# Kernel tuning notes

Measured on AMD Instinct MI355X. Metric: run time of the kernel, lower is better.

## Reference

```python
import jax, jax.numpy as jnp
import numpy as np

N = 50000
IN_CHNL = 128
OUT_CHNL = 64
HEADS = 2
NEG_SLOPE = 0.2  # PyG GATConv default leaky_relu slope


def gat_conv(x, W, a_src, a_dst, bias, edge_index):
    """PyG-style GATConv (concat=True, add_self_loops=True, eval mode).
    x: [N, F_in], W: [F_in, H*C], a_src/a_dst: [H, C], bias: [H*C],
    edge_index: [2, E] (row 0 = src, row 1 = dst)."""
    n = x.shape[0]
    loops = jnp.arange(n, dtype=edge_index.dtype)
    src = jnp.concatenate([edge_index[0], loops])
    dst = jnp.concatenate([edge_index[1], loops])

    h = (x @ W).reshape(n, HEADS, OUT_CHNL)          # [N, H, C]
    s_src = jnp.einsum('nhc,hc->nh', h, a_src)       # [N, H]
    s_dst = jnp.einsum('nhc,hc->nh', h, a_dst)       # [N, H]

    e = s_src[src] + s_dst[dst]                      # [E', H]
    e = jax.nn.leaky_relu(e, NEG_SLOPE)
    # segment softmax over destination neighborhoods
    e_max = jax.ops.segment_max(e, dst, num_segments=n)
    e_max = jnp.where(jnp.isfinite(e_max), e_max, 0.0)
    e_exp = jnp.exp(e - e_max[dst])
    denom = jax.ops.segment_sum(e_exp, dst, num_segments=n)
    alpha = e_exp / denom[dst]                       # [E', H]

    msg = h[src] * alpha[:, :, None]                 # [E', H, C]
    out = jax.ops.segment_sum(msg, dst, num_segments=n)  # [N, H, C]
    return out.reshape(n, HEADS * OUT_CHNL) + bias


def setup_inputs() -> dict:
    key = jax.random.key(0)
    ks = jax.random.split(key, 12)
    node_h = jax.random.normal(ks[0], (N, IN_CHNL), dtype=jnp.float32)
    edge_index_pc = jax.random.randint(ks[1], (2, 600000), 0, N, dtype=jnp.int64 if jax.config.jax_enable_x64 else jnp.int32)
    edge_index_mc = jax.random.randint(ks[2], (2, 600000), 0, N, dtype=jnp.int64 if jax.config.jax_enable_x64 else jnp.int32)
    sc = 1.0 / np.sqrt(IN_CHNL)
    W_pc = jax.random.normal(ks[3], (IN_CHNL, HEADS * OUT_CHNL), dtype=jnp.float32) * sc
    a_src_pc = jax.random.normal(ks[4], (HEADS, OUT_CHNL), dtype=jnp.float32) * sc
    a_dst_pc = jax.random.normal(ks[5], (HEADS, OUT_CHNL), dtype=jnp.float32) * sc
    b_pc = jnp.zeros((HEADS * OUT_CHNL,), dtype=jnp.float32)
    W_mc = jax.random.normal(ks[6], (IN_CHNL, HEADS * OUT_CHNL), dtype=jnp.float32) * sc
    a_src_mc = jax.random.normal(ks[7], (HEADS, OUT_CHNL), dtype=jnp.float32) * sc
    a_dst_mc = jax.random.normal(ks[8], (HEADS, OUT_CHNL), dtype=jnp.float32) * sc
    b_mc = jnp.zeros((HEADS * OUT_CHNL,), dtype=jnp.float32)
    return {
        'node_h': node_h,
        'W_pc': W_pc, 'a_src_pc': a_src_pc, 'a_dst_pc': a_dst_pc, 'b_pc': b_pc,
        'W_mc': W_mc, 'a_src_mc': a_src_mc, 'a_dst_mc': a_dst_mc, 'b_mc': b_mc,
        'edge_index_pc': edge_index_pc, 'edge_index_mc': edge_index_mc,
    }


def reference(node_h, W_pc, a_src_pc, a_dst_pc, b_pc,
              W_mc, a_src_mc, a_dst_mc, b_mc,
              edge_index_pc, edge_index_mc):
    # eval mode: F.dropout is identity
    h_pc = jax.nn.elu(gat_conv(node_h, W_pc, a_src_pc, a_dst_pc, b_pc, edge_index_pc))
    h_mc = jax.nn.elu(gat_conv(node_h, W_mc, a_src_mc, a_dst_mc, b_mc, edge_index_mc))
    return 0.5 * (h_pc + h_mc)
```

## Files before the change

kernel.cpp:

```cpp
#include <hip/hip_runtime.h>
#include <hip/hip_bf16.h>

typedef unsigned int u32;
typedef unsigned short u16;
typedef long long i64;
typedef __bf16 bf16x8 __attribute__((ext_vector_type(8)));
typedef float f32x4 __attribute__((ext_vector_type(4)));

static constexpr int NN = 50000;
static constexpr int FI = 128;
static constexpr int FO = 128;
static constexpr int ER = 600000;
static constexpr int GLAB = 6272;
static constexpr int PROWS = 12544;
static constexpr int DSTRIDE = 38;
static constexpr int NQA = 1280;
static constexpr int ACS = (2 * ER + NQA - 1) / NQA;
static constexpr int NBIN = 128;
static constexpr int RBLK = 784;
static constexpr int LCAP = 24;
static constexpr int QCAPB = 10240;
static constexpr int GEMM_BLK = (NN + 63) / 64;
static constexpr float SLOPE = 0.2f;

__device__ __forceinline__ float bf2f(u16 u) {
  u32 x = ((u32)u) << 16;
  return __builtin_bit_cast(float, x);
}
__device__ __forceinline__ u16 f2bf(float f) {
  u32 u = __builtin_bit_cast(u32, f);
  u32 r = (u + 0x7fffu + ((u >> 16) & 1u)) >> 16;
  return (u16)r;
}
__device__ __forceinline__ float ldf(const void* p, size_t i, int isf32) {
  return isf32 ? ((const float*)p)[i] : bf2f(((const u16*)p)[i]);
}
__device__ __forceinline__ int lde(const void* p, size_t i, int is64) {
  return is64 ? (int)((const i64*)p)[i] : ((const int*)p)[i];
}

__device__ __forceinline__ void passA_body(const void* __restrict__ ei0,
                                           const void* __restrict__ ei1,
                                           int* __restrict__ qcurp,
                                           u32* __restrict__ qbuf, int bid) {
  __shared__ u32 lq[NBIN][LCAP];
  __shared__ int lcnt[NBIN];
  __shared__ int gbase[NBIN];
  __shared__ int s_i64;
  int tid = threadIdx.x;
  if (tid < NBIN) lcnt[tid] = 0;
  if (tid < 64) {
    u32 hi = (tid < 32) ? ((const u32*)ei0)[2 * tid + 1] : 1u;
    unsigned long long b2 = __ballot(hi == 0u);
    if (tid == 0) s_i64 = (__popcll(b2) >= 30) ? 1 : 0;
  }
  __syncthreads();
  int i64f = s_i64;
  int beg = bid * ACS;
  int end = min(beg + ACS, 2 * ER);
  for (int e = beg + tid; e < end; e += 256) {
    int g = e >= ER;
    int ee = e - g * ER;
    const void* ei = g ? ei1 : ei0;
    int d = lde(ei, (size_t)ER + ee, i64f);
    int s = lde(ei, (size_t)ee, i64f);
    s = min(max(s, 0), NN - 1);
    d = min(max(d, 0), NN - 1);
    int p = d & 7;
    int label = (d >> 3) + g * GLAB;
    int r = label / RBLK;
    int bin = p * 16 + r;
    int ll = label - r * RBLK;
    u32 entry = ((u32)s << 16) | (u32)ll;
    int pos = atomicAdd(&lcnt[bin], 1);
    if (pos < LCAP) {
      lq[bin][pos] = entry;
    } else {
      int idx = atomicAdd(&qcurp[bin * 16], 1);
      if (idx < QCAPB) qbuf[(size_t)bin * QCAPB + idx] = entry;
    }
  }
  __syncthreads();
  if (tid < NBIN) {
    int n = min(lcnt[tid], LCAP);
    lcnt[tid] = n;
    gbase[tid] = atomicAdd(&qcurp[tid * 16], n);
  }
  __syncthreads();
  int wv = tid >> 6, lane = tid & 63;
  for (int b = wv; b < NBIN; b += 4) {
    int n = lcnt[b];
    int gb = gbase[b];
    for (int i = lane; i < n; i += 64) {
      int idx = gb + i;
      if (idx < QCAPB) qbuf[(size_t)b * QCAPB + idx] = lq[b][i];
    }
  }
}

__global__ __launch_bounds__(256) void k1(
    const void* __restrict__ W0, const void* __restrict__ W1,
    const u32* __restrict__ x32, const void* __restrict__ ei0,
    const void* __restrict__ ei1, u16* __restrict__ wf,
    int* __restrict__ flags, int* __restrict__ qcurp, u32* __restrict__ qbuf) {
  int bid = blockIdx.x;
  int tid = threadIdx.x;
  if (bid < 16) {
    int lane = tid & 63;
    int chunk = bid * 4 + (tid >> 6);
    u32 e = (x32[lane] >> 23) & 0xffu;
    unsigned long long b1 = __ballot(e >= 118u && e <= 137u);
    int f32i = (__popcll(b1) >= 48) ? 1 : 0;
    int g = chunk >> 5, idx = chunk & 31;
    const void* W = g ? W1 : W0;
    int ks = idx >> 3, cg = idx & 7;
    int k0 = ks * 32 + (lane >> 4) * 8;
    int col = cg * 16 + (lane & 15);
    u16 v[8];
#pragma unroll
    for (int j = 0; j < 8; j++)
      v[j] = f2bf(ldf(W, (size_t)(k0 + j) * FO + col, f32i));
    u32 p0 = (u32)v[0] | ((u32)v[1] << 16);
    u32 p1 = (u32)v[2] | ((u32)v[3] << 16);
    u32 p2 = (u32)v[4] | ((u32)v[5] << 16);
    u32 p3 = (u32)v[6] | ((u32)v[7] << 16);
    *reinterpret_cast<uint4*>(wf + (size_t)(chunk * 64 + lane) * 8) =
        make_uint4(p0, p1, p2, p3);
    if (bid == 0 && tid < 64) {
      u32 hi = (tid < 32) ? ((const u32*)ei0)[2 * tid + 1] : 1u;
      unsigned long long b2 = __ballot(hi == 0u);
      if (tid == 0) {
        flags[0] = f32i;
        flags[1] = (__popcll(b2) >= 30) ? 1 : 0;
      }
    }
    return;
  }
  passA_body(ei0, ei1, qcurp, qbuf, bid - 16);
}

__global__ __launch_bounds__(256) void gemm2(
    const void* __restrict__ x, const u16* __restrict__ wf,
    u16* __restrict__ h0, u16* __restrict__ h1, const void* __restrict__ as0,
    const void* __restrict__ ad0, const void* __restrict__ as1,
    const void* __restrict__ ad1, float* __restrict__ ss,
    float* __restrict__ sd, const int* __restrict__ flags) {
  int f32i = flags[0];
  int g = blockIdx.x >= GEMM_BLK;
  int bid = blockIdx.x - g * GEMM_BLK;
  u16* h = g ? h1 : h0;
  const void* as = g ? as1 : as0;
  const void* ad = g ? ad1 : ad0;
  int tid = threadIdx.x;
  int lane = tid & 63, wv = tid >> 6;
  int rowbase = bid * 64 + wv * 16;
  int arow = rowbase + (lane & 15);
  if (arow >= NN) arow = NN - 1;
  int kg = lane >> 4;

  f32x4 acc[8];
#pragma unroll
  for (int i = 0; i < 8; i++) acc[i] = (f32x4){0.f, 0.f, 0.f, 0.f};

#pragma unroll
  for (int ks = 0; ks < 4; ks++) {
    uint4 q;
    if (f32i) {
      const float* xp = (const float*)x + (size_t)arow * FI + ks * 32 + kg * 8;
      float4 v0 = *reinterpret_cast<const float4*>(xp);
      float4 v1 = *reinterpret_cast<const float4*>(xp + 4);
      q.x = (u32)f2bf(v0.x) | ((u32)f2bf(v0.y) << 16);
      q.y = (u32)f2bf(v0.z) | ((u32)f2bf(v0.w) << 16);
      q.z = (u32)f2bf(v1.x) | ((u32)f2bf(v1.y) << 16);
      q.w = (u32)f2bf(v1.z) | ((u32)f2bf(v1.w) << 16);
    } else {
      q = *reinterpret_cast<const uint4*>((const u16*)x + (size_t)arow * FI +
                                          ks * 32 + kg * 8);
    }
    bf16x8 a = __builtin_bit_cast(bf16x8, q);
#pragma unroll
    for (int cg = 0; cg < 8; cg++) {
      bf16x8 b = __builtin_bit_cast(
          bf16x8, *reinterpret_cast<const uint4*>(
                      wf + (size_t)((g * 32 + ks * 8 + cg) * 64 + lane) * 8));
      acc[cg] = __builtin_amdgcn_mfma_f32_16x16x32_bf16(a, b, acc[cg], 0, 0, 0);
    }
  }
#pragma unroll
  for (int cg = 0; cg < 8; cg++) {
#pragma unroll
    for (int r = 0; r < 4; r++) {
      int orow = rowbase + kg * 4 + r;
      if (orow < NN)
        h[(size_t)orow * FO + cg * 16 + (lane & 15)] = f2bf(acc[cg][r]);
    }
  }
  float sa[2][4], sb[2][4];
#pragma unroll
  for (int i = 0; i < 2; i++)
#pragma unroll
    for (int r = 0; r < 4; r++) {
      sa[i][r] = 0.f;
      sb[i][r] = 0.f;
    }
#pragma unroll
  for (int cg = 0; cg < 8; cg++) {
    int c = cg * 16 + (lane & 15);
    float av = ldf(as, c, f32i);
    float dv = ldf(ad, c, f32i);
    int ih = cg >> 2;
#pragma unroll
    for (int r = 0; r < 4; r++) {
      sa[ih][r] += acc[cg][r] * av;
      sb[ih][r] += acc[cg][r] * dv;
    }
  }
#pragma unroll
  for (int i = 0; i < 2; i++)
#pragma unroll
    for (int r = 0; r < 4; r++)
#pragma unroll
      for (int off = 1; off <= 8; off <<= 1) {
        sa[i][r] += __shfl_xor(sa[i][r], off, 64);
        sb[i][r] += __shfl_xor(sb[i][r], off, 64);
      }
  if ((lane & 15) < 4) {
    int r = lane & 3;
    int row = rowbase + kg * 4 + r;
    if (row < NN) {
      reinterpret_cast<float2*>(ss)[(size_t)g * NN + row] =
          make_float2(sa[0][r], sa[1][r]);
      reinterpret_cast<float2*>(sd)[(size_t)g * NN + row] =
          make_float2(sb[0][r], sb[1][r]);
    }
  }
}

__global__ __launch_bounds__(256) void passB(const int* __restrict__ qcurp,
                                             const u32* __restrict__ qbuf,
                                             int* __restrict__ deg,
                                             u16* __restrict__ slots) {
  __shared__ int ldeg[RBLK];
  __shared__ u16 lslots[RBLK * DSTRIDE];
  int tid = threadIdx.x;
  int bin = blockIdx.x;
  int p = bin >> 4, r = bin & 15;
  for (int i = tid; i < RBLK; i += 256) {
    int lgl = r * RBLK + i;
    int g = lgl >= GLAB;
    int lg = lgl - g * GLAB;
    int dst = (lg << 3) | p;
    if (dst < NN) {
      ldeg[i] = 1;
      lslots[i * DSTRIDE] = (u16)dst;
    } else {
      ldeg[i] = 0;
    }
  }
  __syncthreads();
  int qn = min(qcurp[bin * 16], QCAPB);
  const u32* q = qbuf + (size_t)bin * QCAPB;
  for (int i = tid; i < qn; i += 256) {
    u32 pr = q[i];
    int ll = (int)(pr & 0xffffu);
    int old = atomicAdd(&ldeg[ll], 1);
    if (old < DSTRIDE) lslots[ll * DSTRIDE + old] = (u16)(pr >> 16);
  }
  __syncthreads();
  int rowbase = p * PROWS + r * RBLK;
  for (int i = tid; i < RBLK; i += 256) deg[rowbase + i] = min(ldeg[i], DSTRIDE);
  const u32* ls32 = reinterpret_cast<const u32*>(lslots);
  u32* gs32 = reinterpret_cast<u32*>(slots + (size_t)rowbase * DSTRIDE);
  for (int i = tid; i < RBLK * DSTRIDE / 2; i += 256) gs32[i] = ls32[i];
}

__global__ __launch_bounds__(256) void agg2(
    const u16* __restrict__ h0, const u16* __restrict__ h1,
    const float* __restrict__ ss, const float* __restrict__ sd,
    const int* __restrict__ deg, const u16* __restrict__ slots,
    const void* __restrict__ b0p, const void* __restrict__ b1p,
    void* __restrict__ outp, const int* __restrict__ flags) {
  int f32i = flags[0];
  int tid = threadIdx.x;
  int lane = tid & 63, wv = tid >> 6;
  int half = lane >> 5;
  int c = lane & 31;
  int dst = blockIdx.x * 8 + wv * 2 + half;
  int head = c >> 4;
  int hsh = head << 4;
  int hbase = half << 5;
  float res[2][4];
#pragma unroll
  for (int g = 0; g < 2; g++) {
    const uint2* hw = reinterpret_cast<const uint2*>(g ? h1 : h0);
    const float2* ss2 = reinterpret_cast<const float2*>(ss) + (size_t)g * NN;
    float2 sdv = reinterpret_cast<const float2*>(sd)[(size_t)g * NN + dst];
    int row = (dst & 7) * PROWS + g * GLAB + (dst >> 3);
    int n = min(deg[row], DSTRIDE);
    const u16* srow = slots + (size_t)row * DSTRIDE;
    int n1 = min(n, 32);
    int s1 = 0, s2 = 0;
    u32 pp1 = 0, pp2 = 0;
    float dp0 = 0.f, dp1 = 0.f;
    if (c < n1) {
      s1 = srow[c];
      float2 sv = ss2[s1];
      float e0 = sv.x + sdv.x, e1 = sv.y + sdv.y;
      e0 = (e0 > 0.f) ? e0 : SLOPE * e0;
      e1 = (e1 > 0.f) ? e1 : SLOPE * e1;
      float q0 = __expf(e0), q1 = __expf(e1);
      pp1 = (u32)f2bf(q0) | ((u32)f2bf(q1) << 16);
      dp0 += q0;
      dp1 += q1;
    }
    if (c + 32 < n) {
      s2 = srow[c + 32];
      float2 sv = ss2[s2];
      float e0 = sv.x + sdv.x, e1 = sv.y + sdv.y;
      e0 = (e0 > 0.f) ? e0 : SLOPE * e0;
      e1 = (e1 > 0.f) ? e1 : SLOPE * e1;
      float q0 = __expf(e0), q1 = __expf(e1);
      pp2 = (u32)f2bf(q0) | ((u32)f2bf(q1) << 16);
      dp0 += q0;
      dp1 += q1;
    }
#pragma unroll
    for (int off = 16; off >= 1; off >>= 1) {
      dp0 += __shfl_xor(dp0, off, 32);
      dp1 += __shfl_xor(dp1, off, 32);
    }
    float den = head ? dp1 : dp0;
    float a0 = 0.f, a1 = 0.f, a2 = 0.f, a3 = 0.f;
    int n1full = n1 & ~7;
    for (int b = 0; b < n1full; b += 8) {
      uint2 hv[8];
      float pv[8];
#pragma unroll
      for (int t = 0; t < 8; t++) {
        int sj = __shfl(s1, hbase + b + t, 64);
        u32 pp = __shfl(pp1, hbase + b + t, 64);
        pv[t] = bf2f((u16)(pp >> hsh));
        hv[t] = hw[(size_t)sj * 32 + c];
      }
#pragma unroll
      for (int t = 0; t < 8; t++) {
        a0 += pv[t] * bf2f((u16)hv[t].x);
        a1 += pv[t] * bf2f((u16)(hv[t].x >> 16));
        a2 += pv[t] * bf2f((u16)hv[t].y);
        a3 += pv[t] * bf2f((u16)(hv[t].y >> 16));
      }
    }
    if (n1full < n1) {
      uint2 hv[8];
      float pv[8];
#pragma unroll
      for (int t = 0; t < 8; t++) {
        int jj = (n1full + t < n1) ? (n1full + t) : n1full;
        int sj = __shfl(s1, hbase + jj, 64);
        u32 pp = __shfl(pp1, hbase + jj, 64);
        pv[t] = (n1full + t < n1) ? bf2f((u16)(pp >> hsh)) : 0.f;
        hv[t] = hw[(size_t)sj * 32 + c];
      }
#pragma unroll
      for (int t = 0; t < 8; t++) {
        a0 += pv[t] * bf2f((u16)hv[t].x);
        a1 += pv[t] * bf2f((u16)(hv[t].x >> 16));
        a2 += pv[t] * bf2f((u16)hv[t].y);
        a3 += pv[t] * bf2f((u16)(hv[t].y >> 16));
      }
    }
    if (n > 32) {
      int n2 = n - 32;
      for (int b = 0; b < n2; b += 8) {
        uint2 hv[8];
        float pv[8];
#pragma unroll
        for (int t = 0; t < 8; t++) {
          int jj = (b + t < n2) ? (b + t) : b;
          int sj = __shfl(s2, hbase + jj, 64);
          u32 pp = __shfl(pp2, hbase + jj, 64);
          pv[t] = (b + t < n2) ? bf2f((u16)(pp >> hsh)) : 0.f;
          hv[t] = hw[(size_t)sj * 32 + c];
        }
#pragma unroll
        for (int t = 0; t < 8; t++) {
          a0 += pv[t] * bf2f((u16)hv[t].x);
          a1 += pv[t] * bf2f((u16)(hv[t].x >> 16));
          a2 += pv[t] * bf2f((u16)hv[t].y);
          a3 += pv[t] * bf2f((u16)(hv[t].y >> 16));
        }
      }
    }
    float inv = (den > 0.f) ? 1.0f / den : 0.f;
    const void* bias = g ? b1p : b0p;
    float r0 = a0 * inv + ldf(bias, 4 * c + 0, f32i);
    float r1 = a1 * inv + ldf(bias, 4 * c + 1, f32i);
    float r2 = a2 * inv + ldf(bias, 4 * c + 2, f32i);
    float r3 = a3 * inv + ldf(bias, 4 * c + 3, f32i);
    res[g][0] = (r0 > 0.f) ? r0 : (__expf(r0) - 1.0f);
    res[g][1] = (r1 > 0.f) ? r1 : (__expf(r1) - 1.0f);
    res[g][2] = (r2 > 0.f) ? r2 : (__expf(r2) - 1.0f);
    res[g][3] = (r3 > 0.f) ? r3 : (__expf(r3) - 1.0f);
  }
  float r0 = 0.5f * (res[0][0] + res[1][0]);
  float r1 = 0.5f * (res[0][1] + res[1][1]);
  float r2 = 0.5f * (res[0][2] + res[1][2]);
  float r3 = 0.5f * (res[0][3] + res[1][3]);
  if (f32i) {
    reinterpret_cast<float4*>(outp)[(size_t)dst * 32 + c] =
        make_float4(r0, r1, r2, r3);
  } else {
    uint2 o;
    o.x = (u32)f2bf(r0) | ((u32)f2bf(r1) << 16);
    o.y = (u32)f2bf(r2) | ((u32)f2bf(r3) << 16);
    reinterpret_cast<uint2*>(outp)[(size_t)dst * 32 + c] = o;
  }
}

extern "C" void kernel_launch(void* const* d_in, const int* in_sizes, int n_in,
                              void* d_out, int out_size, void* d_ws, size_t ws_size,
                              hipStream_t stream) {
  (void)in_sizes; (void)n_in; (void)out_size; (void)ws_size;
  const void* x = d_in[0];

  char* base = (char*)d_ws;
  size_t off = 0;
  auto alloc = [&](size_t bytes) -> void* {
    void* p = base + off;
    off = (off + bytes + 255) & ~(size_t)255;
    return p;
  };
  int* flags = (int*)alloc(16);
  int* qcurp = (int*)alloc((size_t)NBIN * 16 * 4);
  u16* h0    = (u16*)alloc((size_t)NN * FO * 2);
  u16* h1    = (u16*)alloc((size_t)NN * FO * 2);
  float* ss  = (float*)alloc((size_t)2 * NN * 2 * 4);
  float* sd  = (float*)alloc((size_t)2 * NN * 2 * 4);
  u16* wf    = (u16*)alloc((size_t)2 * 32 * 64 * 8 * 2);
  int* deg   = (int*)alloc((size_t)8 * PROWS * 4);
  u16* slots = (u16*)alloc((size_t)8 * PROWS * DSTRIDE * 2);
  u32* qbuf  = (u32*)alloc((size_t)NBIN * QCAPB * 4);

  const int AGG_BLK = NN / 8;

  hipMemsetAsync(qcurp, 0, (size_t)NBIN * 16 * 4, stream);
  k1<<<16 + NQA, 256, 0, stream>>>(d_in[1], d_in[5], (const u32*)x, d_in[9],
                                   d_in[10], wf, flags, qcurp, qbuf);
  gemm2<<<2 * GEMM_BLK, 256, 0, stream>>>(x, wf, h0, h1, d_in[2], d_in[3],
                                          d_in[6], d_in[7], ss, sd, flags);
  passB<<<NBIN, 256, 0, stream>>>(qcurp, qbuf, deg, slots);
  agg2<<<AGG_BLK, 256, 0, stream>>>(h0, h1, ss, sd, deg, slots, d_in[4],
                                    d_in[8], d_out, flags);
}
```

Baseline: 141.6 us.

## Fuse edge binning with GEMM into one launch, split weight prep, widen agg unroll

Moves weight fragment conversion, flag detection and queue-counter zeroing into a small prep kernel, which replaces the memset. Edge binning (passA) and the GEMM then run as separate block ranges of a single fused launch so their work can overlap on the GPU. The aggregation gather loop is unrolled 16-wide instead of 8-wide, and the separate full and tail loops are merged into one predicated loop. The wider unroll raises register pressure, and the fused kernel's LDS footprint (sized by passA) may lower occupancy for the GEMM blocks.

Result: no change. 139.4 us (-1.6%).

```diff
diff --git a/kernel.cpp b/kernel.cpp
--- a/kernel.cpp
+++ b/kernel.cpp
@@ -37,6 +37,42 @@
 }
 __device__ __forceinline__ int lde(const void* p, size_t i, int is64) {
   return is64 ? (int)((const i64*)p)[i] : ((const int*)p)[i];
+}
+
+__global__ void wfrag_prep(const void* __restrict__ W0,
+                           const void* __restrict__ W1,
+                           const u32* __restrict__ x,
+                           const u32* __restrict__ ei, u16* __restrict__ wf,
+                           int* __restrict__ flags, int* __restrict__ qcurp) {
+  int lane = threadIdx.x;
+  u32 e = (x[lane] >> 23) & 0xffu;
+  unsigned long long b1 = __ballot(e >= 118u && e <= 137u);
+  int f32i = (__popcll(b1) >= 48) ? 1 : 0;
+  int bid = blockIdx.x;
+  if (bid == 64) {
+    u32 hi = (lane < 32) ? ei[2 * lane + 1] : 1u;
+    unsigned long long b2 = __ballot(hi == 0u);
+    if (lane == 0) {
+      flags[0] = f32i;
+      flags[1] = (__popcll(b2) >= 30) ? 1 : 0;
+    }
+    for (int i = lane; i < NBIN * 16; i += 64) qcurp[i] = 0;
+    return;
+  }
+  int g = bid >> 5, idx = bid & 31;
+  const void* W = g ? W1 : W0;
+  int ks = idx >> 3, cg = idx & 7;
+  int k0 = ks * 32 + (lane >> 4) * 8;
+  int col = cg * 16 + (lane & 15);
+  u16 v[8];
+#pragma unroll
+  for (int j = 0; j < 8; j++) v[j] = f2bf(ldf(W, (size_t)(k0 + j) * FO + col, f32i));
+  u32 p0 = (u32)v[0] | ((u32)v[1] << 16);
+  u32 p1 = (u32)v[2] | ((u32)v[3] << 16);
+  u32 p2 = (u32)v[4] | ((u32)v[5] << 16);
+  u32 p3 = (u32)v[6] | ((u32)v[7] << 16);
+  *reinterpret_cast<uint4*>(wf + (size_t)(bid * 64 + lane) * 8) =
+      make_uint4(p0, p1, p2, p3);
 }
 
 __device__ __forceinline__ void passA_body(const void* __restrict__ ei0,
@@ -98,56 +134,14 @@
   }
 }
 
-__global__ __launch_bounds__(256) void k1(
-    const void* __restrict__ W0, const void* __restrict__ W1,
-    const u32* __restrict__ x32, const void* __restrict__ ei0,
-    const void* __restrict__ ei1, u16* __restrict__ wf,
-    int* __restrict__ flags, int* __restrict__ qcurp, u32* __restrict__ qbuf) {
-  int bid = blockIdx.x;
-  int tid = threadIdx.x;
-  if (bid < 16) {
-    int lane = tid & 63;
-    int chunk = bid * 4 + (tid >> 6);
-    u32 e = (x32[lane] >> 23) & 0xffu;
-    unsigned long long b1 = __ballot(e >= 118u && e <= 137u);
-    int f32i = (__popcll(b1) >= 48) ? 1 : 0;
-    int g = chunk >> 5, idx = chunk & 31;
-    const void* W = g ? W1 : W0;
-    int ks = idx >> 3, cg = idx & 7;
-    int k0 = ks * 32 + (lane >> 4) * 8;
-    int col = cg * 16 + (lane & 15);
-    u16 v[8];
-#pragma unroll
-    for (int j = 0; j < 8; j++)
-      v[j] = f2bf(ldf(W, (size_t)(k0 + j) * FO + col, f32i));
-    u32 p0 = (u32)v[0] | ((u32)v[1] << 16);
-    u32 p1 = (u32)v[2] | ((u32)v[3] << 16);
-    u32 p2 = (u32)v[4] | ((u32)v[5] << 16);
-    u32 p3 = (u32)v[6] | ((u32)v[7] << 16);
-    *reinterpret_cast<uint4*>(wf + (size_t)(chunk * 64 + lane) * 8) =
-        make_uint4(p0, p1, p2, p3);
-    if (bid == 0 && tid < 64) {
-      u32 hi = (tid < 32) ? ((const u32*)ei0)[2 * tid + 1] : 1u;
-      unsigned long long b2 = __ballot(hi == 0u);
-      if (tid == 0) {
-        flags[0] = f32i;
-        flags[1] = (__popcll(b2) >= 30) ? 1 : 0;
-      }
-    }
-    return;
-  }
-  passA_body(ei0, ei1, qcurp, qbuf, bid - 16);
-}
-
-__global__ __launch_bounds__(256) void gemm2(
+__device__ __forceinline__ void gemm_body(
     const void* __restrict__ x, const u16* __restrict__ wf,
     u16* __restrict__ h0, u16* __restrict__ h1, const void* __restrict__ as0,
     const void* __restrict__ ad0, const void* __restrict__ as1,
     const void* __restrict__ ad1, float* __restrict__ ss,
-    float* __restrict__ sd, const int* __restrict__ flags) {
-  int f32i = flags[0];
-  int g = blockIdx.x >= GEMM_BLK;
-  int bid = blockIdx.x - g * GEMM_BLK;
+    float* __restrict__ sd, int f32i, int gb) {
+  int g = gb >= GEMM_BLK;
+  int bid = gb - g * GEMM_BLK;
   u16* h = g ? h1 : h0;
   const void* as = g ? as1 : as0;
   const void* ad = g ? ad1 : ad0;
@@ -233,6 +227,22 @@
       reinterpret_cast<float2*>(sd)[(size_t)g * NN + row] =
           make_float2(sb[0][r], sb[1][r]);
     }
+  }
+}
+
+__global__ __launch_bounds__(256) void fat1(
+    const void* __restrict__ x, const u16* __restrict__ wf,
+    u16* __restrict__ h0, u16* __restrict__ h1, const void* __restrict__ as0,
+    const void* __restrict__ ad0, const void* __restrict__ as1,
+    const void* __restrict__ ad1, float* __restrict__ ss,
+    float* __restrict__ sd, const void* __restrict__ ei0,
+    const void* __restrict__ ei1, int* __restrict__ qcurp,
+    u32* __restrict__ qbuf, const int* __restrict__ flags) {
+  if (blockIdx.x < NQA) {
+    passA_body(ei0, ei1, qcurp, qbuf, blockIdx.x);
+  } else {
+    gemm_body(x, wf, h0, h1, as0, ad0, as1, ad1, ss, sd, flags[0],
+              blockIdx.x - NQA);
   }
 }
 
@@ -331,51 +341,32 @@
     }
     float den = head ? dp1 : dp0;
     float a0 = 0.f, a1 = 0.f, a2 = 0.f, a3 = 0.f;
-    int n1full = n1 & ~7;
-    for (int b = 0; b < n1full; b += 8) {
-      uint2 hv[8];
-      float pv[8];
-#pragma unroll
-      for (int t = 0; t < 8; t++) {
-        int sj = __shfl(s1, hbase + b + t, 64);
-        u32 pp = __shfl(pp1, hbase + b + t, 64);
-        pv[t] = bf2f((u16)(pp >> hsh));
+    for (int b = 0; b < n1; b += 16) {
+      uint2 hv[16];
+      float pv[16];
+#pragma unroll
+      for (int t = 0; t < 16; t++) {
+        int jj = (b + t < n1) ? (b + t) : b;
+        int sj = __shfl(s1, hbase + jj, 64);
+        u32 pp = __shfl(pp1, hbase + jj, 64);
+        pv[t] = (b + t < n1) ? bf2f((u16)(pp >> hsh)) : 0.f;
         hv[t] = hw[(size_t)sj * 32 + c];
       }
 #pragma unroll
-      for (int t = 0; t < 8; t++) {
+      for (int t = 0; t < 16; t++) {
         a0 += pv[t] * bf2f((u16)hv[t].x);
         a1 += pv[t] * bf2f((u16)(hv[t].x >> 16));
         a2 += pv[t] * bf2f((u16)hv[t].y);
         a3 += pv[t] * bf2f((u16)(hv[t].y >> 16));
       }
     }
-    if (n1full < n1) {
-      uint2 hv[8];
-      float pv[8];
-#pragma unroll
-      for (int t = 0; t < 8; t++) {
-        int jj = (n1full + t < n1) ? (n1full + t) : n1full;
-        int sj = __shfl(s1, hbase + jj, 64);
-        u32 pp = __shfl(pp1, hbase + jj, 64);
-        pv[t] = (n1full + t < n1) ? bf2f((u16)(pp >> hsh)) : 0.f;
-        hv[t] = hw[(size_t)sj * 32 + c];
-      }
-#pragma unroll
-      for (int t = 0; t < 8; t++) {
-        a0 += pv[t] * bf2f((u16)hv[t].x);
-        a1 += pv[t] * bf2f((u16)(hv[t].x >> 16));
-        a2 += pv[t] * bf2f((u16)hv[t].y);
-        a3 += pv[t] * bf2f((u16)(hv[t].y >> 16));
-      }
-    }
     if (n > 32) {
       int n2 = n - 32;
-      for (int b = 0; b < n2; b += 8) {
-        uint2 hv[8];
-        float pv[8];
-#pragma unroll
-        for (int t = 0; t < 8; t++) {
+      for (int b = 0; b < n2; b += 16) {
+        uint2 hv[16];
+        float pv[16];
+#pragma unroll
+        for (int t = 0; t < 16; t++) {
           int jj = (b + t < n2) ? (b + t) : b;
           int sj = __shfl(s2, hbase + jj, 64);
           u32 pp = __shfl(pp2, hbase + jj, 64);
@@ -383,7 +374,7 @@
           hv[t] = hw[(size_t)sj * 32 + c];
         }
 #pragma unroll
-        for (int t = 0; t < 8; t++) {
+        for (int t = 0; t < 16; t++) {
           a0 += pv[t] * bf2f((u16)hv[t].x);
           a1 += pv[t] * bf2f((u16)(hv[t].x >> 16));
           a2 += pv[t] * bf2f((u16)hv[t].y);
@@ -443,11 +434,12 @@
 
   const int AGG_BLK = NN / 8;
 
-  hipMemsetAsync(qcurp, 0, (size_t)NBIN * 16 * 4, stream);
-  k1<<<16 + NQA, 256, 0, stream>>>(d_in[1], d_in[5], (const u32*)x, d_in[9],
-                                   d_in[10], wf, flags, qcurp, qbuf);
-  gemm2<<<2 * GEMM_BLK, 256, 0, stream>>>(x, wf, h0, h1, d_in[2], d_in[3],
-                                          d_in[6], d_in[7], ss, sd, flags);
+  wfrag_prep<<<65, 64, 0, stream>>>(d_in[1], d_in[5], (const u32*)x,
+                                    (const u32*)d_in[9], wf, flags, qcurp);
+  fat1<<<NQA + 2 * GEMM_BLK, 256, 0, stream>>>(x, wf, h0, h1, d_in[2], d_in[3],
+                                               d_in[6], d_in[7], ss, sd,
+                                               d_in[9], d_in[10], qcurp, qbuf,
+                                               flags);
   passB<<<NBIN, 256, 0, stream>>>(qcurp, qbuf, deg, slots);
   agg2<<<AGG_BLK, 256, 0, stream>>>(h0, h1, ss, sd, deg, slots, d_in[4],
                                     d_in[8], d_out, flags);
```
